# Kernel optimization log

Hardware: AMD Instinct MI355X
Metric: run time of the kernel (lower is better)

The kernel has to match this reference:

```python
import jax, jax.numpy as jnp
import numpy as np

B, S, E, H = 4, 2048, 1024, 16
D = E // H  # head dim = 64


def setup_inputs() -> dict:
    key = jax.random.key(0)
    ks = jax.random.split(key, 5)
    s = 0.02
    return {
        "x": jax.random.normal(ks[0], (B, S, E), dtype=jnp.float32),
        "Wq": jax.random.normal(ks[1], (E, E), dtype=jnp.float32) * s,
        "Wk": jax.random.normal(ks[2], (E, E), dtype=jnp.float32) * s,
        "Wv": jax.random.normal(ks[3], (E, E), dtype=jnp.float32) * s,
        "Wo": jax.random.normal(ks[4], (E, E), dtype=jnp.float32) * s,
        "bo": jnp.zeros((E,), dtype=jnp.float32),
    }


def reference(x, Wq, Wk, Wv, Wo, bo):
    b, s, e = x.shape
    h, d = H, e // H
    # QKV projections -> [b, h, s, d]
    q = (x @ Wq).reshape(b, s, h, d).transpose(0, 2, 1, 3)
    k = (x @ Wk).reshape(b, s, h, d).transpose(0, 2, 1, 3)
    v = (x @ Wv).reshape(b, s, h, d).transpose(0, 2, 1, 3)
    # scores [b, h, s, s], causal mask with -inf, scaled softmax
    a = jnp.einsum('bhqd,bhkd->bhqk', q, k)
    causal = jnp.tril(jnp.ones((s, s), dtype=bool))  # True where allowed
    a = jnp.where(causal, a, -jnp.inf) / jnp.sqrt(jnp.asarray(d, x.dtype))
    a = jax.nn.softmax(a, axis=-1)
    # dropout p=0.0 (identity in eval)
    y = jnp.einsum('bhqk,bhkd->bhqd', a, v)
    y = y.transpose(0, 2, 1, 3).reshape(b, s, e)
    return y @ Wo + bo
```

## Files before the change

kernel.cpp:

```cpp
#include <hip/hip_runtime.h>

typedef __bf16 bf16x8 __attribute__((ext_vector_type(8)));
typedef float f32x4 __attribute__((ext_vector_type(4)));
typedef float f32x16 __attribute__((ext_vector_type(16)));
typedef unsigned short u16x8 __attribute__((ext_vector_type(8)));
typedef unsigned int u32x4 __attribute__((ext_vector_type(4)));
typedef unsigned int u32x2v __attribute__((ext_vector_type(2)));

#define S_LEN 2048
#define NHEAD 16
#define HDIM  64
#define EMB   1024

__device__ __forceinline__ ushort f2b(float v) {
  union { float f; unsigned u; } x; x.f = v;
  unsigned r = (x.u + 0x7fffu + ((x.u >> 16) & 1u)) >> 16;
  return (ushort)r;
}

__device__ __forceinline__ unsigned pk2(float lo, float hi) {
  union { float f; unsigned u; } a, b; a.f = lo; b.f = hi;
  return (b.u & 0xffff0000u) | (a.u >> 16);
}

typedef const __attribute__((address_space(1))) unsigned int* gp1_t;
typedef __attribute__((address_space(3))) unsigned int* lp3_t;
__device__ __forceinline__ void gld16(const ushort* g, const ushort* l) {
  __builtin_amdgcn_global_load_lds((gp1_t)(unsigned long long)(uintptr_t)g,
                                   (lp3_t)(unsigned int)(uintptr_t)l, 16, 0, 0);
}

__device__ __forceinline__ void barf() {
  asm volatile("" ::: "memory");
  __builtin_amdgcn_s_barrier();
  asm volatile("" ::: "memory");
}

__global__ __launch_bounds__(256) void prep_kernel(
    const float* __restrict__ x, const float* __restrict__ W0,
    const float* __restrict__ W1, const float* __restrict__ W2,
    const float* __restrict__ W3, ushort* __restrict__ xb,
    ushort* __restrict__ Wt0, ushort* __restrict__ Wt1,
    ushort* __restrict__ Wt2, ushort* __restrict__ Wt3, float scale0) {
  const int z = blockIdx.z;
  if (z == 4) {
    size_t base = ((size_t)(blockIdx.y * 32 + blockIdx.x)) * 8192 + threadIdx.x * 4;
#pragma unroll
    for (int i = 0; i < 8; ++i) {
      float4 v = *(const float4*)(x + base + i * 1024);
      ushort4 o;
      o.x = f2b(v.x); o.y = f2b(v.y); o.z = f2b(v.z); o.w = f2b(v.w);
      *(ushort4*)(xb + base + i * 1024) = o;
    }
    return;
  }
  __shared__ float t[32][33];
  const float* W = z == 0 ? W0 : (z == 1 ? W1 : (z == 2 ? W2 : W3));
  ushort* Wt = z == 0 ? Wt0 : (z == 1 ? Wt1 : (z == 2 ? Wt2 : Wt3));
  const float scale = z == 0 ? scale0 : 1.0f;
  int k0 = blockIdx.x * 32, n0 = blockIdx.y * 32;
  int c = threadIdx.x & 31, r0 = threadIdx.x >> 5;
#pragma unroll
  for (int i = 0; i < 4; ++i) {
    int r = r0 + i * 8;
    t[r][c] = W[(size_t)(k0 + r) * EMB + n0 + c];
  }
  __syncthreads();
#pragma unroll
  for (int i = 0; i < 4; ++i) {
    int r = r0 + i * 8;
    Wt[(size_t)(n0 + r) * EMB + k0 + c] = f2b(t[c][r] * scale);
  }
}

__global__ __launch_bounds__(512, 2) void gemm256_kernel(
    const ushort* __restrict__ A, const ushort* __restrict__ Bt,
    ushort* __restrict__ outQ, ushort* __restrict__ outK,
    ushort* __restrict__ outVt) {
  __shared__ ushort lds2[65536];
  const int tid = threadIdx.x;
  const int wave = tid >> 6, lane = tid & 63, ln = lane & 15, quad = lane >> 4;
  const int wm = wave >> 2, wn = wave & 3;
  const long m0 = (long)blockIdx.x * 256, n0 = (long)blockIdx.y * 256;
  constexpr int K = EMB, KT = K / 64;

  const int srow = tid >> 3;
  const int scol = ((tid & 7) ^ (srow & 7)) * 8;
  const ushort* srcA = A + (m0 + srow) * (long)K + scol;
  const ushort* srcB = Bt + (n0 + srow) * (long)K + scol;

#define STG_A(t, b)                                                            \
  do {                                                                         \
    _Pragma("unroll") for (int ld = 0; ld < 4; ++ld)                           \
        gld16(srcA + (t) * 64 + ld * 64 * K,                                   \
              lds2 + (b) * 16384 + ld * 4096 + tid * 8);                       \
  } while (0)
#define STG_B(t, b)                                                            \
  do {                                                                         \
    _Pragma("unroll") for (int ld = 0; ld < 4; ++ld)                           \
        gld16(srcB + (t) * 64 + ld * 64 * K,                                   \
              lds2 + 32768 + (b) * 16384 + ld * 4096 + tid * 8);               \
  } while (0)

  const int sw = (ln & 7) * 8;

#define RD_A8(F, kk, b)                                                        \
  do {                                                                         \
    const ushort* p_ = lds2 + (b) * 16384 + (wm * 128 + ln) * 64 +             \
                       (((kk) * 32 + quad * 8) ^ sw);                          \
    _Pragma("unroll") for (int m_ = 0; m_ < 8; ++m_)                           \
        F[m_] = *(const bf16x8*)(p_ + m_ * 1024);                              \
  } while (0)
#define RD_B4(F, kk, b)                                                        \
  do {                                                                         \
    const ushort* p_ = lds2 + 32768 + (b) * 16384 + (wn * 64 + ln) * 64 +      \
                       (((kk) * 32 + quad * 8) ^ sw);                          \
    _Pragma("unroll") for (int n_ = 0; n_ < 4; ++n_)                           \
        F[n_] = *(const bf16x8*)(p_ + n_ * 1024);                              \
  } while (0)

#define MM32(AF, BF)                                                           \
  do {                                                                         \
    __builtin_amdgcn_s_setprio(1);                                             \
    _Pragma("unroll") for (int mt = 0; mt < 8; ++mt)                           \
        _Pragma("unroll") for (int nt = 0; nt < 4; ++nt)                       \
            acc[mt][nt] = __builtin_amdgcn_mfma_f32_16x16x32_bf16(             \
                AF[mt], BF[nt], acc[mt][nt], 0, 0, 0);                         \
    __builtin_amdgcn_s_setprio(0);                                             \
  } while (0)

  f32x4 acc[8][4] = {};
  bf16x8 afP[8], bfP[4], afN[8], bfN[4];

  STG_A(0, 0); STG_B(0, 0);
  asm volatile("s_waitcnt vmcnt(0)" ::: "memory");
  barf();

  for (int kt = 0; kt < KT; ++kt) {
    const int bb = kt & 1;
    if (kt + 1 < KT) { STG_A(kt + 1, bb ^ 1); STG_B(kt + 1, bb ^ 1); }
    RD_A8(afP, 0, bb); RD_B4(bfP, 0, bb);
    MM32(afP, bfP);
    RD_A8(afN, 1, bb); RD_B4(bfN, 1, bb);
    MM32(afN, bfN);
    if (kt + 1 < KT) {
      asm volatile("s_waitcnt vmcnt(0) lgkmcnt(0)" ::: "memory");
      barf();
    }
  }

  const int sel = (int)(n0 >> 10);
  if (sel == 2) {
#pragma unroll
    for (int mt = 0; mt < 8; ++mt) {
      const long mbase = m0 + wm * 128 + mt * 16 + quad * 4;
      const long bb2 = mbase >> 11, s = mbase & 2047;
#pragma unroll
      for (int nt = 0; nt < 4; ++nt) {
        const int nn = (int)((n0 & 1023) + wn * 64 + nt * 16 + ln);
        const int h = nn >> 6, d = nn & 63;
        uint2 val;
        val.x = (unsigned)f2b(acc[mt][nt][0]) | ((unsigned)f2b(acc[mt][nt][1]) << 16);
        val.y = (unsigned)f2b(acc[mt][nt][2]) | ((unsigned)f2b(acc[mt][nt][3]) << 16);
        *(uint2*)(outVt + (((bb2 * NHEAD + h) * (long)HDIM + d) * S_LEN) + s) = val;
      }
    }
  } else {
    ushort* dst = sel == 0 ? outQ : outK;
#pragma unroll
    for (int mt = 0; mt < 8; ++mt) {
#pragma unroll
      for (int nt = 0; nt < 4; ++nt) {
        const int nn = (int)((n0 & 1023) + wn * 64 + nt * 16 + ln);
        const int h = nn >> 6, d = nn & 63;
#pragma unroll
        for (int r = 0; r < 4; ++r) {
          const long m = m0 + wm * 128 + mt * 16 + quad * 4 + r;
          const long bb2 = m >> 11, s = m & 2047;
          dst[(((bb2 * NHEAD + h) * S_LEN) + s) * HDIM + d] = f2b(acc[mt][nt][r]);
        }
      }
    }
  }
#undef MM32
#undef RD_B4
#undef RD_A8
#undef STG_B
#undef STG_A
}

template <int EPI>
__global__ __launch_bounds__(512, 2) void gemm8_kernel(
    const ushort* __restrict__ A, const ushort* __restrict__ Bt,
    float* __restrict__ outF, const float* __restrict__ bias) {
  __shared__ ushort lds8[73728];
  const int tid = threadIdx.x;
  const int wave = tid >> 6, lane = tid & 63, ln = lane & 15, quad = lane >> 4;
  const int wm = wave >> 2, wn = wave & 3;
  const long m0 = (long)blockIdx.x * 128, n0 = (long)blockIdx.y * 256;
  constexpr int K = EMB, KT = K / 64;

  const int srow = tid >> 3;
  const int scol = ((tid & 7) ^ (srow & 7)) * 8;
  const ushort* srcA = A + (m0 + srow) * (long)K + scol;
  const ushort* srcB = Bt + (n0 + srow) * (long)K + scol;

#define STG_A(t, s)                                                            \
  do {                                                                         \
    gld16(srcA + (t) * 64,               lds8 + (s) * 8192 + tid * 8);         \
    gld16(srcA + (t) * 64 + 64 * K,      lds8 + (s) * 8192 + 4096 + tid * 8);  \
  } while (0)
#define STG_B(t, s)                                                            \
  do {                                                                         \
    gld16(srcB + (t) * 64,               lds8 + 24576 + (s) * 16384 + tid * 8);         \
    gld16(srcB + (t) * 64 + 64 * K,      lds8 + 24576 + (s) * 16384 + 4096 + tid * 8);  \
    gld16(srcB + (t) * 64 + 128 * K,     lds8 + 24576 + (s) * 16384 + 8192 + tid * 8);  \
    gld16(srcB + (t) * 64 + 192 * K,     lds8 + 24576 + (s) * 16384 + 12288 + tid * 8); \
  } while (0)

  const int sw = (ln & 7) * 8;

#define RD_A(F, kk, s)                                                         \
  do {                                                                         \
    const ushort* p_ = lds8 + (s) * 8192 + (wm * 64 + ln) * 64 +               \
                       (((kk) * 32 + quad * 8) ^ sw);                          \
    F[0] = *(const bf16x8*)p_;                                                 \
    F[1] = *(const bf16x8*)(p_ + 1024);                                        \
    F[2] = *(const bf16x8*)(p_ + 2048);                                        \
    F[3] = *(const bf16x8*)(p_ + 3072);                                        \
  } while (0)
#define RD_B(F, kk, s)                                                         \
  do {                                                                         \
    const ushort* p_ = lds8 + 24576 + (s) * 16384 + (wn * 64 + ln) * 64 +      \
                       (((kk) * 32 + quad * 8) ^ sw);                          \
    F[0] = *(const bf16x8*)p_;                                                 \
    F[1] = *(const bf16x8*)(p_ + 1024);                                        \
    F[2] = *(const bf16x8*)(p_ + 2048);                                        \
    F[3] = *(const bf16x8*)(p_ + 3072);                                        \
  } while (0)

#define MM16(AF, BF)                                                           \
  do {                                                                         \
    __builtin_amdgcn_s_setprio(1);                                             \
    _Pragma("unroll") for (int mt = 0; mt < 4; ++mt)                           \
        _Pragma("unroll") for (int nt = 0; nt < 4; ++nt)                       \
            acc[mt][nt] = __builtin_amdgcn_mfma_f32_16x16x32_bf16(             \
                AF[mt], BF[nt], acc[mt][nt], 0, 0, 0);                         \
    __builtin_amdgcn_s_setprio(0);                                             \
  } while (0)

  f32x4 acc[4][4] = {};
  bf16x8 afP[4], bfP[4], afN[4], bfN[4];

  STG_A(0, 0); STG_B(0, 0);
  STG_A(1, 1); STG_B(1, 1);
  asm volatile("s_waitcnt vmcnt(6)" ::: "memory");
  barf();
  RD_A(afP, 0, 0); RD_B(bfP, 0, 0);

#define TILE_FULL(t, s, s1, s2)                                                \
  do {                                                                         \
    STG_A((t) + 2, s2);                                                        \
    RD_A(afN, 1, s); RD_B(bfN, 1, s);                                          \
    MM16(afP, bfP);                                                            \
    STG_B((t) + 2, s2);                                                        \
    asm volatile("s_waitcnt vmcnt(6) lgkmcnt(0)" ::: "memory");                \
    barf();                                                                    \
    RD_A(afP, 0, s1); RD_B(bfP, 0, s1);                                        \
    MM16(afN, bfN);                                                            \
  } while (0)

  for (int th = 0; th < 12; th += 3) {
    TILE_FULL(th, 0, 1, 2);
    TILE_FULL(th + 1, 1, 2, 0);
    TILE_FULL(th + 2, 2, 0, 1);
  }
  TILE_FULL(12, 0, 1, 2);
  TILE_FULL(13, 1, 2, 0);
  RD_A(afN, 1, 2); RD_B(bfN, 1, 2);
  MM16(afP, bfP);
  asm volatile("s_waitcnt vmcnt(0) lgkmcnt(0)" ::: "memory");
  barf();
  RD_A(afP, 0, 0); RD_B(bfP, 0, 0);
  MM16(afN, bfN);
  RD_A(afN, 1, 0); RD_B(bfN, 1, 0);
  MM16(afP, bfP);
  MM16(afN, bfN);

#pragma unroll
  for (int mt = 0; mt < 4; ++mt) {
#pragma unroll
    for (int nt = 0; nt < 4; ++nt) {
      const long n = n0 + wn * 64 + nt * 16 + ln;
      const float bv = bias[n];
#pragma unroll
      for (int r = 0; r < 4; ++r) {
        const long m = m0 + wm * 64 + mt * 16 + quad * 4 + r;
        outF[m * (long)EMB + n] = acc[mt][nt][r] + bv;
      }
    }
  }
#undef TILE_FULL
#undef MM16
#undef RD_B
#undef RD_A
#undef STG_B
#undef STG_A
}

__global__ __launch_bounds__(256, 3) void attn_kernel(const ushort* __restrict__ Q,
                                                      const ushort* __restrict__ Kg,
                                                      const ushort* __restrict__ Vt,
                                                      ushort* __restrict__ Y) {
  __shared__ alignas(16) ushort Ks[3][4096];
  __shared__ alignas(16) ushort Vs[3][4096];
  const int tid = threadIdx.x;
  const int wave = tid >> 6, lane = tid & 63;
  const int l31 = lane & 31, hi = lane >> 5;
  const int bh = blockIdx.x;
  const int qb = 15 - (int)blockIdx.y;
  const int q0 = qb * 128;
  const size_t base = (size_t)bh * S_LEN * HDIM;
  const int ntiles = 2 * qb + 2;

  const u16x8 ob = {0x3F80, 0x3F80, 0x3F80, 0x3F80, 0x3F80, 0x3F80, 0x3F80, 0x3F80};
  const bf16x8 ones = __builtin_bit_cast(bf16x8, ob);

  bf16x8 qf[4];
#pragma unroll
  for (int dsub = 0; dsub < 4; ++dsub)
    qf[dsub] = *(const bf16x8*)(Q + base + (size_t)(q0 + wave * 32 + l31) * HDIM +
                                dsub * 16 + hi * 8);

  f32x16 acc0 = {}, acc1 = {}, accl = {};

  const int srow = tid >> 3;
  const int scc  = ((tid & 7) ^ (srow & 7)) * 8;
  const ushort* KgS = Kg + base + (size_t)srow * HDIM + scc;
  const ushort* VgS = Vt + base + (size_t)srow * S_LEN + scc;

#define STAGE(t, s)                                                            \
  do {                                                                         \
    const size_t kk_ = (size_t)(t) * 64;                                       \
    gld16(KgS + kk_ * HDIM,               &Ks[s][0] + tid * 8);                \
    gld16(KgS + (kk_ + 32) * HDIM,        &Ks[s][0] + 2048 + tid * 8);         \
    gld16(VgS + kk_,                      &Vs[s][0] + tid * 8);                \
    gld16(VgS + 32 * (size_t)S_LEN + kk_, &Vs[s][0] + 2048 + tid * 8);         \
  } while (0)

  STAGE(0, 0);
  STAGE(1, 1);
  asm volatile("s_waitcnt vmcnt(4)" ::: "memory");
  barf();

  const int swL = (lane & 7) * 8;
  const int qbase = q0 + wave * 32;
  int sc = 0, sn = 1, ss = 2;

  for (int kt = 0; kt < ntiles; ++kt) {
    const int k0 = kt * 64;
    const bool do_stage = (kt + 2 < ntiles);
    if (do_stage) STAGE(kt + 2, ss);

    const ushort* Kc = &Ks[sc][0];
    const ushort* Vc = &Vs[sc][0];

    if (k0 < qbase + 32) {
      f32x16 sT0 = {}, sT1 = {};
      __builtin_amdgcn_s_setprio(1);
#pragma unroll
      for (int dsub = 0; dsub < 4; ++dsub) {
        const int c = (dsub * 16 + hi * 8) ^ swL;
        bf16x8 kf0 = *(const bf16x8*)(Kc + l31 * 64 + c);
        bf16x8 kf1 = *(const bf16x8*)(Kc + (32 + l31) * 64 + c);
        sT0 = __builtin_amdgcn_mfma_f32_32x32x16_bf16(kf0, qf[dsub], sT0, 0, 0, 0);
        sT1 = __builtin_amdgcn_mfma_f32_32x32x16_bf16(kf1, qf[dsub], sT1, 0, 0, 0);
      }
      __builtin_amdgcn_s_setprio(0);

      if (k0 + 63 > qbase) {
        const int rowq = qbase + l31;
#pragma unroll
        for (int r = 0; r < 16; ++r) {
          const int key = k0 + ((r & 3) + 8 * (r >> 2)) + 4 * hi;
          if (key > rowq) sT0[r] = -3.0e38f;
          if (key + 32 > rowq) sT1[r] = -3.0e38f;
        }
      }

      unsigned pw0[8], pw1[8];
#pragma unroll
      for (int i = 0; i < 8; ++i) {
        pw0[i] = pk2(__builtin_amdgcn_exp2f(sT0[2 * i]),
                     __builtin_amdgcn_exp2f(sT0[2 * i + 1]));
        pw1[i] = pk2(__builtin_amdgcn_exp2f(sT1[2 * i]),
                     __builtin_amdgcn_exp2f(sT1[2 * i + 1]));
      }

#define KEYBLK(PW, KSQ0)                                                       \
  do {                                                                         \
    u32x2v r02 = __builtin_amdgcn_permlane32_swap(PW[0], PW[2], false, false); \
    u32x2v r13 = __builtin_amdgcn_permlane32_swap(PW[1], PW[3], false, false); \
    u32x2v r46 = __builtin_amdgcn_permlane32_swap(PW[4], PW[6], false, false); \
    u32x2v r57 = __builtin_amdgcn_permlane32_swap(PW[5], PW[7], false, false); \
    u32x4 fwA, fwB;                                                            \
    fwA[0] = r02[0]; fwA[1] = r13[0]; fwA[2] = r02[1]; fwA[3] = r13[1];        \
    fwB[0] = r46[0]; fwB[1] = r57[0]; fwB[2] = r46[1]; fwB[3] = r57[1];        \
    bf16x8 paA = __builtin_bit_cast(bf16x8, fwA);                              \
    bf16x8 paB = __builtin_bit_cast(bf16x8, fwB);                              \
    __builtin_amdgcn_s_setprio(1);                                             \
    accl = __builtin_amdgcn_mfma_f32_32x32x16_bf16(paA, ones, accl, 0, 0, 0);  \
    accl = __builtin_amdgcn_mfma_f32_32x32x16_bf16(paB, ones, accl, 0, 0, 0);  \
    {                                                                          \
      const int vcA = (((KSQ0)) * 16 + hi * 8) ^ swL;                          \
      bf16x8 va0 = *(const bf16x8*)(Vc + l31 * 64 + vcA);                      \
      bf16x8 va1 = *(const bf16x8*)(Vc + (32 + l31) * 64 + vcA);               \
      acc0 = __builtin_amdgcn_mfma_f32_32x32x16_bf16(paA, va0, acc0, 0, 0, 0); \
      acc1 = __builtin_amdgcn_mfma_f32_32x32x16_bf16(paA, va1, acc1, 0, 0, 0); \
      const int vcB = (((KSQ0) + 1) * 16 + hi * 8) ^ swL;                      \
      bf16x8 vb0 = *(const bf16x8*)(Vc + l31 * 64 + vcB);                      \
      bf16x8 vb1 = *(const bf16x8*)(Vc + (32 + l31) * 64 + vcB);               \
      acc0 = __builtin_amdgcn_mfma_f32_32x32x16_bf16(paB, vb0, acc0, 0, 0, 0); \
      acc1 = __builtin_amdgcn_mfma_f32_32x32x16_bf16(paB, vb1, acc1, 0, 0, 0); \
    }                                                                          \
    __builtin_amdgcn_s_setprio(0);                                             \
  } while (0)

      KEYBLK(pw0, 0);
      KEYBLK(pw1, 2);
#undef KEYBLK
    }

    if (kt + 1 < ntiles) {
      if (do_stage) {
        asm volatile("s_waitcnt vmcnt(4) lgkmcnt(0)" ::: "memory");
      } else {
        asm volatile("s_waitcnt vmcnt(0) lgkmcnt(0)" ::: "memory");
      }
      barf();
    }
    const int t_ = sc; sc = sn; sn = ss; ss = t_;
  }
#undef STAGE

  const long b = bh >> 4;
  const int h = bh & 15;
#pragma unroll
  for (int r = 0; r < 16; ++r) {
    const float inv = 1.0f / accl[r];
    const int qq = q0 + wave * 32 + ((r & 3) + 8 * (r >> 2)) + 4 * hi;
    ushort* yp = Y + (((b * S_LEN + qq) * NHEAD) + h) * HDIM;
    yp[l31]      = f2b(acc0[r] * inv);
    yp[32 + l31] = f2b(acc1[r] * inv);
  }
}

extern "C" void kernel_launch(void* const* d_in, const int* in_sizes, int n_in,
                              void* d_out, int out_size, void* d_ws, size_t ws_size,
                              hipStream_t stream) {
  const float* x  = (const float*)d_in[0];
  const float* Wq = (const float*)d_in[1];
  const float* Wk = (const float*)d_in[2];
  const float* Wv = (const float*)d_in[3];
  const float* Wo = (const float*)d_in[4];
  const float* bo = (const float*)d_in[5];
  float* out = (float*)d_out;

  const size_t XE = (size_t)8192 * EMB;
  ushort* ws    = (ushort*)d_ws;
  ushort* xb    = ws;
  ushort* Wtqkv = xb + XE;
  ushort* Wto   = Wtqkv + 3 * 1048576;
  ushort* Qb    = Wto + 1048576;
  ushort* Kb    = Qb + XE;
  ushort* Vtb   = Kb + XE;
  ushort* Yb    = xb;

  const float SCALE_Q = 1.4426950408889634f / 8.0f;

  prep_kernel<<<dim3(32, 32, 5), 256, 0, stream>>>(
      x, Wq, Wk, Wv, Wo, xb, Wtqkv, Wtqkv + 1048576, Wtqkv + 2097152, Wto, SCALE_Q);

  gemm256_kernel<<<dim3(32, 12), 512, 0, stream>>>(xb, Wtqkv, Qb, Kb, Vtb);
  attn_kernel<<<dim3(64, 16), 256, 0, stream>>>(Qb, Kb, Vtb, Yb);
  gemm8_kernel<1><<<dim3(64, 4), 512, 0, stream>>>(Yb, Wto, out, bo);
}
```

Before: 232.1 us.

## Software-pipeline LDS fragment reads in QKV GEMM and shrink attention V buffering

In the QKV GEMM, LDS fragment reads are moved ahead of the MFMA blocks so the next half-tile reads overlap the current matmul, and the next tile's first fragments are read right after the barrier. In attention, V staging becomes double-buffered (prefetched one tile ahead) while K stays triple-buffered. This cuts LDS use from 48KB to 40KB so launch bounds can request 4 blocks per CU instead of 3. The trade-off is less prefetch distance for V and more register pressure under the tighter occupancy target. An unused template parameter on the output GEMM is also dropped.

```diff
diff --git a/kernel.cpp b/kernel.cpp
--- a/kernel.cpp
+++ b/kernel.cpp
@@ -135,18 +135,19 @@
   STG_A(0, 0); STG_B(0, 0);
   asm volatile("s_waitcnt vmcnt(0)" ::: "memory");
   barf();
+  RD_A8(afP, 0, 0); RD_B4(bfP, 0, 0);
 
   for (int kt = 0; kt < KT; ++kt) {
     const int bb = kt & 1;
     if (kt + 1 < KT) { STG_A(kt + 1, bb ^ 1); STG_B(kt + 1, bb ^ 1); }
-    RD_A8(afP, 0, bb); RD_B4(bfP, 0, bb);
+    RD_A8(afN, 1, bb); RD_B4(bfN, 1, bb);
     MM32(afP, bfP);
-    RD_A8(afN, 1, bb); RD_B4(bfN, 1, bb);
-    MM32(afN, bfN);
     if (kt + 1 < KT) {
       asm volatile("s_waitcnt vmcnt(0) lgkmcnt(0)" ::: "memory");
       barf();
-    }
+      RD_A8(afP, 0, bb ^ 1); RD_B4(bfP, 0, bb ^ 1);
+    }
+    MM32(afN, bfN);
   }
 
   const int sel = (int)(n0 >> 10);
@@ -189,7 +190,6 @@
 #undef STG_A
 }
 
-template <int EPI>
 __global__ __launch_bounds__(512, 2) void gemm8_kernel(
     const ushort* __restrict__ A, const ushort* __restrict__ Bt,
     float* __restrict__ outF, const float* __restrict__ bias) {
@@ -308,12 +308,12 @@
 #undef STG_A
 }
 
-__global__ __launch_bounds__(256, 3) void attn_kernel(const ushort* __restrict__ Q,
+__global__ __launch_bounds__(256, 4) void attn_kernel(const ushort* __restrict__ Q,
                                                       const ushort* __restrict__ Kg,
                                                       const ushort* __restrict__ Vt,
                                                       ushort* __restrict__ Y) {
   __shared__ alignas(16) ushort Ks[3][4096];
-  __shared__ alignas(16) ushort Vs[3][4096];
+  __shared__ alignas(16) ushort Vs[2][4096];
   const int tid = threadIdx.x;
   const int wave = tid >> 6, lane = tid & 63;
   const int l31 = lane & 31, hi = lane >> 5;
@@ -339,18 +339,23 @@
   const ushort* KgS = Kg + base + (size_t)srow * HDIM + scc;
   const ushort* VgS = Vt + base + (size_t)srow * S_LEN + scc;
 
-#define STAGE(t, s)                                                            \
+#define STAGE_K(t, s)                                                          \
   do {                                                                         \
     const size_t kk_ = (size_t)(t) * 64;                                       \
     gld16(KgS + kk_ * HDIM,               &Ks[s][0] + tid * 8);                \
     gld16(KgS + (kk_ + 32) * HDIM,        &Ks[s][0] + 2048 + tid * 8);         \
-    gld16(VgS + kk_,                      &Vs[s][0] + tid * 8);                \
-    gld16(VgS + 32 * (size_t)S_LEN + kk_, &Vs[s][0] + 2048 + tid * 8);         \
-  } while (0)
-
-  STAGE(0, 0);
-  STAGE(1, 1);
-  asm volatile("s_waitcnt vmcnt(4)" ::: "memory");
+  } while (0)
+#define STAGE_V(t, b)                                                          \
+  do {                                                                         \
+    const size_t kk_ = (size_t)(t) * 64;                                       \
+    gld16(VgS + kk_,                      &Vs[b][0] + tid * 8);                \
+    gld16(VgS + 32 * (size_t)S_LEN + kk_, &Vs[b][0] + 2048 + tid * 8);         \
+  } while (0)
+
+  STAGE_K(0, 0);
+  STAGE_V(0, 0);
+  STAGE_K(1, 1);
+  asm volatile("s_waitcnt vmcnt(2)" ::: "memory");
   barf();
 
   const int swL = (lane & 7) * 8;
@@ -359,11 +364,14 @@
 
   for (int kt = 0; kt < ntiles; ++kt) {
     const int k0 = kt * 64;
-    const bool do_stage = (kt + 2 < ntiles);
-    if (do_stage) STAGE(kt + 2, ss);
+    const int vbuf = kt & 1;
+    const bool stV = (kt + 1 < ntiles);
+    const bool stK = (kt + 2 < ntiles);
+    if (stV) STAGE_V(kt + 1, vbuf ^ 1);
+    if (stK) STAGE_K(kt + 2, ss);
 
     const ushort* Kc = &Ks[sc][0];
-    const ushort* Vc = &Vs[sc][0];
+    const ushort* Vc = &Vs[vbuf][0];
 
     if (k0 < qbase + 32) {
       f32x16 sT0 = {}, sT1 = {};
@@ -432,8 +440,8 @@
     }
 
     if (kt + 1 < ntiles) {
-      if (do_stage) {
-        asm volatile("s_waitcnt vmcnt(4) lgkmcnt(0)" ::: "memory");
+      if (stK) {
+        asm volatile("s_waitcnt vmcnt(2) lgkmcnt(0)" ::: "memory");
       } else {
         asm volatile("s_waitcnt vmcnt(0) lgkmcnt(0)" ::: "memory");
       }
@@ -441,7 +449,8 @@
     }
     const int t_ = sc; sc = sn; sn = ss; ss = t_;
   }
-#undef STAGE
+#undef STAGE_V
+#undef STAGE_K
 
   const long b = bh >> 4;
   const int h = bh & 15;
@@ -483,5 +492,5 @@
 
   gemm256_kernel<<<dim3(32, 12), 512, 0, stream>>>(xb, Wtqkv, Qb, Kb, Vtb);
   attn_kernel<<<dim3(64, 16), 256, 0, stream>>>(Qb, Kb, Vtb, Yb);
-  gemm8_kernel<1><<<dim3(64, 4), 512, 0, stream>>>(Yb, Wto, out, bo);
-}
+  gemm8_kernel<<<dim3(64, 4), 512, 0, stream>>>(Yb, Wto, out, bo);
+}
```

Result: faster. 223.0 us (-3.9%).
